# Optimization experiments

Measured on AMD Instinct MI355X. Metric: run time of the kernel, lower is better.

## Reference

```python
import jax, jax.numpy as jnp
import numpy as np

B, T, D, H = 8, 1024, 512, 8
QD, PD, POSD, VD, K = 32, 4, 48, 64, 31
FF = 4 * D
FF1, FF2, FF3, NLA = FF * 3 // 4, FF, FF * 5 // 4, D * 3 // 4


def _swoosh_l(x):
    return jax.nn.softplus(x - 4.0) - 0.08 * x - 0.035


def _swoosh_r(x):
    return jax.nn.softplus(x - 1.0) - 0.08 * x - 0.313261687


def setup_inputs() -> dict:
    key = jax.random.key(0)
    ks = iter(jax.random.split(key, 64))

    def w(shape, fan_in):
        return jax.random.normal(next(ks), shape, jnp.float32) * (fan_in ** -0.5)

    inp = {
        'x': jax.random.normal(next(ks), (B, T, D), jnp.float32),
        'pos_emb': jax.random.normal(next(ks), (2 * T - 1, POSD), jnp.float32),
        'mask': jnp.ones((B, T), bool),
        'attw_q_w': w((D, H * QD), D), 'attw_k_w': w((D, H * QD), D),
        'attw_pq_w': w((D, H * PD), D), 'attw_pos_w': w((POSD, H * PD), POSD),
        'ff1_in_w': w((D, FF1), D), 'ff1_in_b': jnp.zeros(FF1),
        'ff1_out_w': w((FF1, D), FF1), 'ff1_out_b': jnp.zeros(D),
        'nla_w': w((D, NLA * 3), D), 'nla_b': jnp.zeros(NLA * 3),
        'nla_out_w': w((NLA, D), NLA), 'nla_out_b': jnp.zeros(D),
        'sa1_v_w': w((D, H * VD), D), 'sa1_v_b': jnp.zeros(H * VD),
        'sa1_o_w': w((H * VD, D), H * VD), 'sa1_o_b': jnp.zeros(D),
        'conv1_in_w': w((D, 2 * D), D), 'conv1_in_b': jnp.zeros(2 * D),
        'conv1_dw_w': w((D, 1, K), K), 'conv1_dw_b': jnp.zeros(D),
        'conv1_out_w': w((D, D), D), 'conv1_out_b': jnp.zeros(D),
        'ff2_in_w': w((D, FF2), D), 'ff2_in_b': jnp.zeros(FF2),
        'ff2_out_w': w((FF2, D), FF2), 'ff2_out_b': jnp.zeros(D),
        'mid_scale': jax.random.uniform(next(ks), (D,), jnp.float32),
        'sa2_v_w': w((D, H * VD), D), 'sa2_v_b': jnp.zeros(H * VD),
        'sa2_o_w': w((H * VD, D), H * VD), 'sa2_o_b': jnp.zeros(D),
        'conv2_in_w': w((D, 2 * D), D), 'conv2_in_b': jnp.zeros(2 * D),
        'conv2_dw_w': w((D, 1, K), K), 'conv2_dw_b': jnp.zeros(D),
        'conv2_out_w': w((D, D), D), 'conv2_out_b': jnp.zeros(D),
        'ff3_in_w': w((D, FF3), D), 'ff3_in_b': jnp.zeros(FF3),
        'ff3_out_w': w((FF3, D), FF3), 'ff3_out_b': jnp.zeros(D),
        'norm_bias': jnp.zeros(D), 'norm_log_scale': jnp.zeros(()),
        'out_scale': jax.random.uniform(next(ks), (D,), jnp.float32),
    }
    return inp


def _forward(x, pos_emb, attw_q_w, attw_k_w, attw_pq_w, attw_pos_w,
             ff1_in_w, ff1_in_b, ff1_out_w, ff1_out_b,
             nla_w, nla_b, nla_out_w, nla_out_b,
             sa1_v_w, sa1_v_b, sa1_o_w, sa1_o_b,
             conv1_in_w, conv1_in_b, conv1_dw_w, conv1_dw_b, conv1_out_w, conv1_out_b,
             ff2_in_w, ff2_in_b, ff2_out_w, ff2_out_b,
             mid_scale,
             sa2_v_w, sa2_v_b, sa2_o_w, sa2_o_b,
             conv2_in_w, conv2_in_b, conv2_dw_w, conv2_dw_b, conv2_out_w, conv2_out_b,
             ff3_in_w, ff3_in_b, ff3_out_w, ff3_out_b,
             norm_bias, norm_log_scale, out_scale, mask):
    res = x
    # --- relative-pos multi-head attention weights ---
    q = (x @ attw_q_w).reshape(B, T, H, QD).transpose(0, 2, 1, 3)
    k = (x @ attw_k_w).reshape(B, T, H, QD).transpose(0, 2, 1, 3)
    p = (x @ attw_pq_w).reshape(B, T, H, PD).transpose(0, 2, 1, 3)
    content = jnp.einsum('bhtd,bhsd->bhts', q, k) * (QD ** -0.5)
    rel = (pos_emb @ attw_pos_w).reshape(2 * T - 1, H, PD).transpose(1, 0, 2)
    idx = jnp.arange(T)[:, None] - jnp.arange(T)[None, :] + (T - 1)
    relg = rel[:, idx]  # [H, T, T, PD]
    scores = content + jnp.einsum('bhtd,htsd->bhts', p, relg)
    scores = jnp.where(mask[:, None, None, :], scores, -10000.0)
    attn = jax.nn.softmax(scores, axis=-1)
    attn = jnp.where(mask[:, None, :, None], attn, 0.0)

    def mk(y):
        return jnp.where(mask[..., None], y, 0.0)

    def ff(y, wi, bi, wo, bo):
        return _swoosh_l(y @ wi + bi) @ wo + bo

    def sa(y, vw, vb, ow, ob):
        v = (y @ vw + vb).reshape(B, T, H, VD).transpose(0, 2, 1, 3)
        o = jnp.einsum('bhts,bhsd->bhtd', attn, v).transpose(0, 2, 1, 3).reshape(B, T, H * VD)
        return o @ ow + ob

    def conv(y, iw, ib, dw, db, ow, ob):
        u = y @ iw + ib
        a, g = jnp.split(u, 2, axis=-1)
        a = (a * jax.nn.sigmoid(g)).transpose(0, 2, 1)  # [B, D, T]
        a = jnp.where(mask[:, None, :], a, 0.0)
        c = jax.lax.conv_general_dilated(a, dw, (1,), [(K // 2, K // 2)],
                                         dimension_numbers=('NCH', 'OIH', 'NCH'),
                                         feature_group_count=D) + db[None, :, None]
        c = _swoosh_r(c.transpose(0, 2, 1))
        return mk(c @ ow + ob)

    def bypass(r, u, s):
        s = jnp.clip(s, 0.2, 1.0)  # eval/steady regime
        return r + (u - r) * s

    x = mk(x + ff(x, ff1_in_w, ff1_in_b, ff1_out_w, ff1_out_b))
    # non-linear attention (uses head 0)
    a, b, c = jnp.split(x @ nla_w + nla_b, 3, axis=-1)
    att0 = jnp.einsum('bts,bsd->btd', attn[:, 0], jnp.tanh(b) * c)
    x = mk(x + ((a * att0) @ nla_out_w + nla_out_b))
    x = mk(x + sa(x, sa1_v_w, sa1_v_b, sa1_o_w, sa1_o_b))
    x = mk(x + conv(x, conv1_in_w, conv1_in_b, conv1_dw_w, conv1_dw_b, conv1_out_w, conv1_out_b))
    x = mk(x + ff(x, ff2_in_w, ff2_in_b, ff2_out_w, ff2_out_b))
    x = mk(bypass(res, x, mid_scale))
    x = mk(x + sa(x, sa2_v_w, sa2_v_b, sa2_o_w, sa2_o_b))
    x = mk(x + conv(x, conv2_in_w, conv2_in_b, conv2_dw_w, conv2_dw_b, conv2_out_w, conv2_out_b))
    x = mk(x + ff(x, ff3_in_w, ff3_in_b, ff3_out_w, ff3_out_b))
    # BiasNorm
    rms = jnp.sqrt(jnp.mean((x - norm_bias) ** 2, axis=-1, keepdims=True) + 1e-8)
    x = x / rms * jnp.exp(norm_log_scale)
    x = mk(bypass(res, x, out_scale))
    return x


def reference(x, pos_emb, mask, attw_q_w, attw_k_w, attw_pq_w, attw_pos_w,
              ff1_in_w, ff1_in_b, ff1_out_w, ff1_out_b,
              nla_w, nla_b, nla_out_w, nla_out_b,
              sa1_v_w, sa1_v_b, sa1_o_w, sa1_o_b,
              conv1_in_w, conv1_in_b, conv1_dw_w, conv1_dw_b, conv1_out_w, conv1_out_b,
              ff2_in_w, ff2_in_b, ff2_out_w, ff2_out_b,
              mid_scale,
              sa2_v_w, sa2_v_b, sa2_o_w, sa2_o_b,
              conv2_in_w, conv2_in_b, conv2_dw_w, conv2_dw_b, conv2_out_w, conv2_out_b,
              ff3_in_w, ff3_in_b, ff3_out_w, ff3_out_b,
              norm_bias, norm_log_scale, out_scale):
    return _forward(x, pos_emb, attw_q_w, attw_k_w, attw_pq_w, attw_pos_w,
                    ff1_in_w, ff1_in_b, ff1_out_w, ff1_out_b,
                    nla_w, nla_b, nla_out_w, nla_out_b,
                    sa1_v_w, sa1_v_b, sa1_o_w, sa1_o_b,
                    conv1_in_w, conv1_in_b, conv1_dw_w, conv1_dw_b, conv1_out_w, conv1_out_b,
                    ff2_in_w, ff2_in_b, ff2_out_w, ff2_out_b,
                    mid_scale,
                    sa2_v_w, sa2_v_b, sa2_o_w, sa2_o_b,
                    conv2_in_w, conv2_in_b, conv2_dw_w, conv2_dw_b, conv2_out_w, conv2_out_b,
                    ff3_in_w, ff3_in_b, ff3_out_w, ff3_out_b,
                    norm_bias, norm_log_scale, out_scale, mask)
```

## Files before the change

kernel.cpp:

```cpp
#include <hip/hip_runtime.h>
#include <hip/hip_bf16.h>
#include <math.h>

using bf16 = __hip_bfloat16;
using f16 = _Float16;
typedef short s16x8 __attribute__((ext_vector_type(8)));
typedef f16   f16x2 __attribute__((ext_vector_type(2)));
typedef float f32x4 __attribute__((ext_vector_type(4)));
typedef unsigned int u32;
#define DEV __device__ __forceinline__
#define AS1 __attribute__((address_space(1)))
#define AS3 __attribute__((address_space(3)))

constexpr int Bc = 8, Tc = 1024, Dc = 512, Hc = 8;
constexpr int QDc = 32, PDc = 4, POSDc = 48, VDc = 64;
constexpr int Nrow = Bc * Tc;
constexpr int KWc = 31;

DEV float frcp(float x) { return __builtin_amdgcn_rcpf(x); }
DEV float softplus_f(float y) { return fmaxf(y, 0.f) + __logf(1.f + __expf(-fabsf(y))); }
DEV float swoosh_l_f(float x) { return softplus_f(x - 4.f) - 0.08f * x - 0.035f; }
DEV float swoosh_r_f(float x) { return softplus_f(x - 1.f) - 0.08f * x - 0.313261687f; }
DEV float sigmoid_f(float x)  { return frcp(1.f + __expf(-x)); }
DEV float tanh_f(float x) {
// ... 9 lines not shown
DEV u32 packbf(float a, float b) {
  return ((u32)(unsigned short)f2bb(b) << 16) | (u32)(unsigned short)f2bb(a);
}
DEV float dot2(u32 a, u32 b, float c) {
#if __has_builtin(__builtin_amdgcn_fdot2)
  union { u32 u; f16x2 v; } x, y; x.u = a; y.u = b;
  return __builtin_amdgcn_fdot2(x.v, y.v, c, false);
#else
  return c + h2f(a & 0xffff) * h2f(b & 0xffff) + h2f(a >> 16) * h2f(b >> 16);
#endif
}

DEV float wave_max(float v) {
#pragma unroll
  for (int o = 32; o > 0; o >>= 1) v = fmaxf(v, __shfl_xor(v, o));
  return v;
}
DEV float wave_sum(float v) {
#pragma unroll
  for (int o = 32; o > 0; o >>= 1) v += __shfl_xor(v, o);
  return v;
}

DEV void gload16(const void* g, void* l) {
  __builtin_amdgcn_global_load_lds((const AS1 u32*)g, (AS3 u32*)l, 16, 0, 0);
}

#define SWZ(a) ((a) ^ ((((a) >> 7) & 7) << 4))

template <int ACT, int WM, int WN, int FM, int FN>
__global__ __launch_bounds__(256) void gemm_mfma(
    const bf16* __restrict__ A, const bf16* __restrict__ B,
    const float* __restrict__ bias, const float* __restrict__ resid,
    float* __restrict__ Cf, bf16* __restrict__ Cb,
    int M, int N, int K, int lda, int ldb, int ldc,
    long sAz, long sBo, long sBi, long sCo, long sCi, int nh) {
  constexpr int BM = WM * FM * 16, BN = WN * FN * 16;
  constexpr int ASZ = BM * 128, BUF = (BM + BN) * 128;
  constexpr int LPS = BM / 32 + BN / 32;

  int z = blockIdx.z;
  int zo = z / nh, zi = z - zo * nh;
  A += (long)z * sAz;
  B += (long)zo * sBo + (long)zi * sBi;
  long coff = (long)zo * sCo + (long)zi * sCi;

  __shared__ char lds[2 * BUF];

  int tid = threadIdx.x;
  int lane = tid & 63, w = tid >> 6;
  int wm = w / WN, wn = w % WN;

  int gx = gridDim.x;
  int nwg = gx * gridDim.y;
  int flat = blockIdx.y * gx + blockIdx.x;
  if ((nwg & 7) == 0) flat = (flat & 7) * (nwg >> 3) + (flat >> 3);
  int m0 = (flat / gx) * BM, n0 = (flat % gx) * BN;

  int lrow = lane >> 3, lch = lane & 7;
  const bf16* ga = A + (long)(m0 + w * (BM / 4) + lrow) * lda + ((lch ^ lrow) << 3);
  const bf16* gb = B + (long)(n0 + w * (BN / 4) + lrow) * ldb + ((lch ^ lrow) << 3);

  f32x4 acc[FM][FN];
#pragma unroll
  for (int i = 0; i < FM; ++i)
#pragma unroll
    for (int j = 0; j < FN; ++j) acc[i][j] = 0.f;

  int nt = K >> 6;
  {
    char* la = lds + w * (BM / 4) * 128;
    char* lb = lds + ASZ + w * (BN / 4) * 128;
#pragma unroll
    for (int i = 0; i < BM / 32; ++i) gload16(ga + (long)(i * 8) * lda, la + i * 1024);
#pragma unroll
    for (int i = 0; i < BN / 32; ++i) gload16(gb + (long)(i * 8) * ldb, lb + i * 1024);
  }

  for (int t = 0; t < nt; ++t) {
    char* cA = lds + (t & 1) * BUF;
    char* cB = cA + ASZ;
    if (t + 1 < nt) {
      int k0 = (t + 1) << 6;
      char* la = lds + ((t + 1) & 1) * BUF + w * (BM / 4) * 128;
      char* lb = lds + ((t + 1) & 1) * BUF + ASZ + w * (BN / 4) * 128;
#pragma unroll
      for (int i = 0; i < BM / 32; ++i) gload16(ga + (long)(i * 8) * lda + k0, la + i * 1024);
#pragma unroll
      for (int i = 0; i < BN / 32; ++i) gload16(gb + (long)(i * 8) * ldb + k0, lb + i * 1024);
      asm volatile("s_waitcnt vmcnt(%0)" :: "n"(LPS) : "memory");
    } else {
      asm volatile("s_waitcnt vmcnt(0)" ::: "memory");
    }
    __builtin_amdgcn_s_barrier();
    __builtin_amdgcn_sched_barrier(0);
#pragma unroll
    for (int ks = 0; ks < 2; ++ks) {
      int cg = ks * 4 + (lane >> 4);
      s16x8 af[FM], bfr[FN];
#pragma unroll
      for (int f = 0; f < FM; ++f) {
        int row = wm * FM * 16 + f * 16 + (lane & 15);
        af[f] = *(const s16x8*)(cA + row * 128 + ((cg ^ (row & 7)) << 4));
      }
#pragma unroll
      for (int f = 0; f < FN; ++f) {
        int row = wn * FN * 16 + f * 16 + (lane & 15);
        bfr[f] = *(const s16x8*)(cB + row * 128 + ((cg ^ (row & 7)) << 4));
      }
#pragma unroll
      for (int fm = 0; fm < FM; ++fm)
#pragma unroll
        for (int fn = 0; fn < FN; ++fn)
          acc[fm][fn] = __builtin_amdgcn_mfma_f32_16x16x32_bf16(
              af[fm], bfr[fn], acc[fm][fn], 0, 0, 0);
    }
    __builtin_amdgcn_sched_barrier(0);
    __builtin_amdgcn_s_barrier();
  }

  int rbase = m0 + wm * FM * 16 + (lane >> 4) * 4;
  int cbase = n0 + wn * FN * 16 + (lane & 15);
#pragma unroll
  for (int fn = 0; fn < FN; ++fn) {
    int col = cbase + fn * 16;
    if (col >= N) continue;
    float bv = bias ? bias[col] : 0.f;
#pragma unroll
    for (int fm = 0; fm < FM; ++fm) {
#pragma unroll
      for (int r = 0; r < 4; ++r) {
        int row = rbase + fm * 16 + r;
        if (row >= M) continue;
        float v = acc[fm][fn][r] + bv;
        if (ACT == 1) v = swoosh_l_f(v);
        long ci = coff + (long)row * ldc + col;
        if (resid) v += resid[ci];
        if (Cf) Cf[ci] = v;
        if (Cb) Cb[ci] = __float2bfloat16(v);
      }
    }
  }
}

__global__ __launch_bounds__(256) void gemm_mfma_nt(
    const bf16* __restrict__ A, const bf16* __restrict__ B,
    bf16* __restrict__ Cb, int M, int N, int K, int lda, int ldb, int ldc,
    long sAz, long sBo, long sCo) {
  int z = blockIdx.z;
  A += (long)z * sAz;
  B += (long)z * sBo;
  long coff = (long)z * sCo;

  __shared__ char lds[32768];
  char* Al = lds;
  char* Bl = lds + 16384;

  int tid = threadIdx.x;
  int lane = tid & 63, w = tid >> 6;
  int wm = w >> 1, wn = w & 1;
  int m0 = blockIdx.y * 128, n0 = blockIdx.x * 128;

  f32x4 acc[4][4];
#pragma unroll
  for (int i = 0; i < 4; ++i)
#pragma unroll
    for (int j = 0; j < 4; ++j) acc[i][j] = 0.f;

  for (int k0 = 0; k0 < K; k0 += 64) {
#pragma unroll
    for (int i = 0; i < 4; ++i) {
      int flat = tid + i * 256;
// ... 164 lines not shown
  for (int e = 0; e < 8; ++e) o1[e] = t[q * 16 + 8 + e][j];
  short* dp = (short*)dst + (long)(by + j) * R + bx + q * 16;
  *(s16x8*)dp = o0;
  *(s16x8*)(dp + 8) = o1;
}

__global__ void dw_transpose_kernel(const float* __restrict__ dw1, float* __restrict__ o1,
                                    const float* __restrict__ dw2, float* __restrict__ o2) {
  int i = blockIdx.x * 256 + threadIdx.x;
  if (i >= 2 * 512 * KWc) return;
  const float* s = (i < 512 * KWc) ? dw1 : dw2;
  float* o = (i < 512 * KWc) ? o1 : o2;
  int j = (i < 512 * KWc) ? i : i - 512 * KWc;
  int d = j / KWc, kk = j - d * KWc;
  o[kk * 512 + d] = s[j];
}

__global__ void f2b_kernel(const float* __restrict__ in, bf16* __restrict__ out, int nOct) {
  int i = blockIdx.x * 256 + threadIdx.x;
  if (i >= nOct) return;
  float4 a = *(const float4*)(in + (long)i * 8);
  float4 b = *(const float4*)(in + (long)i * 8 + 4);
  s16x8 o;
  o[0] = f2bb(a.x); o[1] = f2bb(a.y); o[2] = f2bb(a.z); o[3] = f2bb(a.w);
  o[4] = f2bb(b.x); o[5] = f2bb(b.y); o[6] = f2bb(b.z); o[7] = f2bb(b.w);
  *(s16x8*)((short*)out + (long)i * 8) = o;
}

__global__ __launch_bounds__(256) void scores_softmax_fused(
    const bf16* __restrict__ qk, const f16* __restrict__ ph,
    const float* __restrict__ rel, bf16* __restrict__ attn) {
  int bh = blockIdx.y;
  int h = bh & (Hc - 1), b = bh >> 3;
  int t0 = blockIdx.x * 32;
  int tid = threadIdx.x, lane = tid & 63, w = tid >> 6;
  int wr = w >> 1, wc = w & 1;

  __shared__ unsigned short scS[32 * 1024];
  __shared__ u32 rel01[1056], rel23[1056];
  __shared__ u32 pS[32][2];
  __shared__ float mS[32][2], lS[32][2];

  for (int i = tid; i < 1055; i += 256) {
    float4 rv = *(const float4*)(rel + (long)(t0 + i) * 32 + h * 4);
    rel01[i] = ((u32)f2h(rv.y) << 16) | f2h(rv.x);
    rel23[i] = ((u32)f2h(rv.w) << 16) | f2h(rv.z);
  }
  if (tid < 32) {
    const u32* pp = (const u32*)(ph + ((long)(b * Tc + t0 + tid)) * 32 + h * 4);
    pS[tid][0] = pp[0]; pS[tid][1] = pp[1];
  }

  s16x8 af = *(const s16x8*)(qk + ((long)(b * Tc + t0 + wr * 16 + (lane & 15))) * 512 +
                             h * QDc + (lane >> 4) * 8);
  int g = lane >> 4;
  int r0 = wr * 16 + g * 4;
  float mx[4] = {-3e38f, -3e38f, -3e38f, -3e38f};
  f32x4 zero = {0.f, 0.f, 0.f, 0.f};
#pragma unroll 4
  for (int tile = 0; tile < 32; ++tile) {
    int s0 = wc * 512 + tile * 16;
    s16x8 bfr = *(const s16x8*)(qk + ((long)(b * Tc + s0 + (lane & 15))) * 512 +
                                256 + h * QDc + (lane >> 4) * 8);
    f32x4 acc = __builtin_amdgcn_mfma_f32_16x16x32_bf16(af, bfr, zero, 0, 0, 0);
    int scol = s0 + (lane & 15);
#pragma unroll
    for (int r = 0; r < 4; ++r) {
      float v = acc[r];
      mx[r] = fmaxf(mx[r], v);
      int trow = r0 + r;
      int byteoff = trow * 2048 + ((scol * 2) ^ (((trow >> 2) & 3) << 5));
      *(unsigned short*)((char*)scS + byteoff) = f2h(v);
    }
  }
#pragma unroll
  for (int o = 1; o < 16; o <<= 1)
#pragma unroll
    for (int r = 0; r < 4; ++r) mx[r] = fmaxf(mx[r], __shfl_xor(mx[r], o));
  if ((lane & 15) == 0) {
#pragma unroll
    for (int r = 0; r < 4; ++r) mS[r0 + r][wc] = mx[r];
  }
  __syncthreads();

  for (int r = 0; r < 16; ++r) {
    int trow = wr * 16 + r;
    float mf = fmaxf(mS[trow][0], mS[trow][1]);
    u32 p01 = pS[trow][0], p23 = pS[trow][1];
    int mask = ((trow >> 2) & 3) << 5;
    char* rowbase = (char*)scS + trow * 2048;
    float lsum = 0.f;
#pragma unroll
    for (int i = 0; i < 4; ++i) {
      int byteoff = (wc * 1024 + lane * 4 + i * 256) ^ mask;
      u32 cw = *(u32*)(rowbase + byteoff);
      int scol0 = wc * 512 + (lane + i * 64) * 2;
      int i0 = trow - scol0 + 1023;
      float pos0 = dot2(p23, rel23[i0],     dot2(p01, rel01[i0],     0.f));
      float pos1 = dot2(p23, rel23[i0 - 1], dot2(p01, rel01[i0 - 1], 0.f));
      float e0 = __expf(h2f(cw & 0xffff) + pos0 - mf);
      float e1 = __expf(h2f(cw >> 16)    + pos1 - mf);
      lsum += e0 + e1;
      *(u32*)(rowbase + byteoff) = packbf(e0, e1);
    }
    lsum = wave_sum(lsum);
    if (lane == 0) lS[trow][wc] = lsum;
  }
  __syncthreads();

  for (int r = 0; r < 16; ++r) {
    int trow = wr * 16 + r;
    float inv = frcp(lS[trow][0] + lS[trow][1]);
    int mask = ((trow >> 2) & 3) << 5;
    char* rowbase = (char*)scS + trow * 2048;
    u32* grow = (u32*)(attn + ((long)bh * Tc + t0 + trow) * Tc) + wc * 256;
#pragma unroll
    for (int i = 0; i < 4; ++i) {
      int byteoff = (wc * 1024 + lane * 4 + i * 256) ^ mask;
      u32 ew = *(u32*)(rowbase + byteoff);
      grow[lane + i * 64] = packbf(b2f((short)(ew & 0xffff)) * inv,
                                   b2f((short)(ew >> 16)) * inv);
    }
  }
}

__global__ void glu_kernel(const bf16* __restrict__ u, bf16* __restrict__ out, int nOct) {
  int i = blockIdx.x * 256 + threadIdx.x;
  if (i >= nOct) return;
  int row = i >> 6, oct = i & 63;
  const short* ur = (const short*)u + (long)row * 1024;
  s16x8 av = *(const s16x8*)(ur + oct * 8);
  s16x8 gv = *(const s16x8*)(ur + 512 + oct * 8);
  s16x8 o;
#pragma unroll
  for (int j = 0; j < 8; ++j) o[j] = f2bb(b2f(av[j]) * sigmoid_f(b2f(gv[j])));
  *(s16x8*)((short*)out + (long)row * 512 + oct * 8) = o;
}

__global__ void tanhmul_kernel(const bf16* __restrict__ abc, bf16* __restrict__ out, int nOct) {
  int i = blockIdx.x * 256 + threadIdx.x;
  if (i >= nOct) return;
  int row = i / 48, oct = i - row * 48;
  const short* r = (const short*)abc + (long)row * 1152;
  s16x8 bv = *(const s16x8*)(r + 384 + oct * 8);
  s16x8 cv = *(const s16x8*)(r + 768 + oct * 8);
  s16x8 o;
#pragma unroll
  for (int j = 0; j < 8; ++j) o[j] = f2bb(tanh_f(b2f(bv[j])) * b2f(cv[j]));
  *(s16x8*)((short*)out + (long)row * 384 + oct * 8) = o;
}

__global__ void amul_kernel(const bf16* __restrict__ abc, bf16* __restrict__ io, int nOct) {
  int i = blockIdx.x * 256 + threadIdx.x;
  if (i >= nOct) return;
  int row = i / 48, oct = i - row * 48;
  const short* r = (const short*)abc + (long)row * 1152;
  s16x8 av = *(const s16x8*)(r + oct * 8);
  short* p = (short*)io + (long)row * 384 + oct * 8;
  s16x8 v = *(const s16x8*)p;
#pragma unroll
  for (int j = 0; j < 8; ++j) v[j] = f2bb(b2f(v[j]) * b2f(av[j]));
  *(s16x8*)p = v;
}

__global__ void bypass_kernel(const float* __restrict__ r, const float* __restrict__ u,
                              const float* __restrict__ s, float* __restrict__ out,
                              bf16* __restrict__ outb, int nOct) {
  int i = blockIdx.x * 256 + threadIdx.x;
  if (i >= nOct) return;
  int d0 = (i & 63) * 8;
  long base = (long)i * 8;
  float4 r0 = *(const float4*)(r + base), r1 = *(const float4*)(r + base + 4);
  float4 u0 = *(const float4*)(u + base), u1 = *(const float4*)(u + base + 4);
  float4 s0 = *(const float4*)(s + d0),  s1 = *(const float4*)(s + d0 + 4);
  float4 o0, o1;
  o0.x = r0.x + (u0.x - r0.x) * clip_s(s0.x);
  o0.y = r0.y + (u0.y - r0.y) * clip_s(s0.y);
  o0.z = r0.z + (u0.z - r0.z) * clip_s(s0.z);
  o0.w = r0.w + (u0.w - r0.w) * clip_s(s0.w);
  o1.x = r1.x + (u1.x - r1.x) * clip_s(s1.x);
  o1.y = r1.y + (u1.y - r1.y) * clip_s(s1.y);
  o1.z = r1.z + (u1.z - r1.z) * clip_s(s1.z);
  o1.w = r1.w + (u1.w - r1.w) * clip_s(s1.w);
  *(float4*)(out + base) = o0;
  *(float4*)(out + base + 4) = o1;
  s16x8 ob;
  ob[0] = f2bb(o0.x); ob[1] = f2bb(o0.y); ob[2] = f2bb(o0.z); ob[3] = f2bb(o0.w);
  ob[4] = f2bb(o1.x); ob[5] = f2bb(o1.y); ob[6] = f2bb(o1.z); ob[7] = f2bb(o1.w);
  *(s16x8*)((short*)outb + base) = ob;
}

// ... 27 lines not shown
  *(s16x8*)((short*)c + (long)bt * 512 + oct * 8) = o;
}

__global__ __launch_bounds__(256) void rmsnorm_bypass_kernel(
    const float* __restrict__ x, const float* __restrict__ x0,
    const float* __restrict__ nb, const float* __restrict__ nls,
    const float* __restrict__ os, float* __restrict__ out) {
  int row = blockIdx.x;
  int tid = threadIdx.x;
  const float* xr = x + (long)row * 512;
  const float* rr = x0 + (long)row * 512;
  float* orow = out + (long)row * 512;
  float v0 = xr[tid], v1 = xr[tid + 256];
  float d0 = v0 - nb[tid], d1 = v1 - nb[tid + 256];
  float ss = d0 * d0 + d1 * d1;
  __shared__ float red[4];
  int lane = tid & 63, wid = tid >> 6;
  ss = wave_sum(ss);
  if (lane == 0) red[wid] = ss;
  __syncthreads();
  ss = red[0] + red[1] + red[2] + red[3];
  float rms = sqrtf(ss * (1.f / 512.f) + 1e-8f);
  float scl = expf(nls[0]) / rms;
  float r0 = rr[tid], s0 = clip_s(os[tid]);
  orow[tid] = r0 + (v0 * scl - r0) * s0;
  float r1 = rr[tid + 256], s1 = clip_s(os[tid + 256]);
  orow[tid + 256] = r1 + (v1 * scl - r1) * s1;
}

static inline int cdiv(int a, int b) { return (a + b - 1) / b; }

template <int ACT, int WM = 2, int WN = 2, int FM = 2, int FN = 2>
static void mfma_launch(hipStream_t st, const bf16* A, const bf16* B, const float* bias,
                        const float* resid, float* Cf, bf16* Cb,
                        int M, int N, int K, int lda, int ldb, int ldc,
                        int Z = 1, int nh = 1, long sAz = 0, long sBo = 0, long sBi = 0,
                        long sCo = 0, long sCi = 0) {
  dim3 grid(cdiv(N, WN * FN * 16), cdiv(M, WM * FM * 16), Z);
  gemm_mfma<ACT, WM, WN, FM, FN><<<grid, dim3(256), 0, st>>>(
      A, B, bias, resid, Cf, Cb, M, N, K, lda, ldb, ldc,
      sAz, sBo, sBi, sCo, sCi, nh);
}
#define MFMA_AV 4, 1, 2, 4

extern "C" void kernel_launch(void* const* d_in, const int* in_sizes, int n_in,
                              void* d_out, int out_size, void* d_ws, size_t ws_size,
                              hipStream_t stream) {
  const float* x0        = (const float*)d_in[0];
  const float* pos_emb   = (const float*)d_in[1];
  const float* Wq        = (const float*)d_in[3];
  const float* Wk        = (const float*)d_in[4];
  const float* Wpq       = (const float*)d_in[5];
  const float* Wpos      = (const float*)d_in[6];
  const float* ff1_in_w  = (const float*)d_in[7];
  const float* ff1_in_b  = (const float*)d_in[8];
  const float* ff1_out_w = (const float*)d_in[9];
  const float* ff1_out_b = (const float*)d_in[10];
  const float* nla_w     = (const float*)d_in[11];
  const float* nla_b     = (const float*)d_in[12];
  const float* nla_out_w = (const float*)d_in[13];
  const float* nla_out_b = (const float*)d_in[14];
  const float* sa1_v_w   = (const float*)d_in[15];
  const float* sa1_v_b   = (const float*)d_in[16];
  const float* sa1_o_w   = (const float*)d_in[17];
  const float* sa1_o_b   = (const float*)d_in[18];
  const float* cv1_in_w  = (const float*)d_in[19];
  const float* cv1_in_b  = (const float*)d_in[20];
  const float* cv1_dw_w  = (const float*)d_in[21];
  const float* cv1_dw_b  = (const float*)d_in[22];
  const float* cv1_out_w = (const float*)d_in[23];
  const float* cv1_out_b = (const float*)d_in[24];
  const float* ff2_in_w  = (const float*)d_in[25];
  const float* ff2_in_b  = (const float*)d_in[26];
// ... 4 lines not shown
  const float* sa2_v_b   = (const float*)d_in[31];
  const float* sa2_o_w   = (const float*)d_in[32];
  const float* sa2_o_b   = (const float*)d_in[33];
  const float* cv2_in_w  = (const float*)d_in[34];
  const float* cv2_in_b  = (const float*)d_in[35];
  const float* cv2_dw_w  = (const float*)d_in[36];
  const float* cv2_dw_b  = (const float*)d_in[37];
  const float* cv2_out_w = (const float*)d_in[38];
  const float* cv2_out_b = (const float*)d_in[39];
  const float* ff3_in_w  = (const float*)d_in[40];
  const float* ff3_in_b  = (const float*)d_in[41];
  const float* ff3_out_w = (const float*)d_in[42];
  const float* ff3_out_b = (const float*)d_in[43];
  const float* norm_bias = (const float*)d_in[44];
  const float* nls       = (const float*)d_in[45];
  const float* out_scale = (const float*)d_in[46];
  float* out = (float*)d_out;

  char* wsb = (char*)d_ws;
  size_t off = 0;
  bf16* attn  = (bf16*)(wsb + off); off += (size_t)Bc * Hc * Tc * Tc * 2;
  float* xA   = (float*)(wsb + off); off += (size_t)Nrow * Dc * 4;
  float* xB   = (float*)(wsb + off); off += (size_t)Nrow * Dc * 4;
  bf16*  xb   = (bf16*)(wsb + off);  off += (size_t)Nrow * Dc * 2;
  bf16*  x0b  = (bf16*)(wsb + off);  off += (size_t)Nrow * Dc * 2;
  bf16*  big1b = (bf16*)(wsb + off); off += (size_t)Nrow * 2560 * 2;
  bf16*  big2b = (bf16*)(wsb + off); off += (size_t)Nrow * Dc * 2;
  bf16*  wT    = (bf16*)(wsb + off); off += (size_t)9961472 * 2;
  float* dwT1  = (float*)(wsb + off); off += (size_t)KWc * 512 * 4;
  float* dwT2  = (float*)(wsb + off); off += (size_t)KWc * 512 * 4;
  bf16* big3b = big1b + (size_t)Nrow * 2048;
  bf16* vT    = big2b;
  bf16* qk    = big1b;
  f16*  ph    = (f16*)(big1b + (size_t)Nrow * 512);
  float* relb = (float*)(ph + (size_t)Nrow * 32);

  bf16* p_w = wT;
  auto alloc_w = [&](int n, int k) { bf16* r = p_w; p_w += (size_t)n * k; return r; };
  bf16* ff1_in_wT  = alloc_w(1536, 512);
  bf16* ff1_out_wT = alloc_w(512, 1536);
  bf16* nla_wT     = alloc_w(1152, 512);
  bf16* nla_out_wT = alloc_w(512, 384);
  bf16* sa1_v_wT   = alloc_w(512, 512);
  bf16* sa1_o_wT   = alloc_w(512, 512);
  bf16* cv1_in_wT  = alloc_w(1024, 512);
  bf16* cv1_out_wT = alloc_w(512, 512);
  bf16* ff2_in_wT  = alloc_w(2048, 512);
  bf16* ff2_out_wT = alloc_w(512, 2048);
  bf16* sa2_v_wT   = alloc_w(512, 512);
  bf16* sa2_o_wT   = alloc_w(512, 512);
  bf16* cv2_in_wT  = alloc_w(1024, 512);
  bf16* cv2_out_wT = alloc_w(512, 512);
  bf16* ff3_in_wT  = alloc_w(2560, 512);
  bf16* ff3_out_wT = alloc_w(512, 2560);
  bf16* WqkT       = alloc_w(512, 512);

  const int nOctD  = Nrow * 64;
  const int nOct384 = Nrow * 48;

  f2b_kernel<<<cdiv(nOctD, 256), 256, 0, stream>>>(x0, x0b, nOctD);
  {
    TBatch tb{};
    auto add = [&](int idx, const float* s, bf16* d, int K, int N, int& t0, float sc) {
      tb.d[idx] = {s, d, K, N, t0, cdiv(N, 32), sc};
      t0 += cdiv(N, 32) * cdiv(K, 32);
    };
    int t0 = 0;
    add(0,  ff1_in_w,  ff1_in_wT,  512, 1536, t0, 1.f);
    add(1,  ff1_out_w, ff1_out_wT, 1536, 512, t0, 1.f);
    add(2,  nla_w,     nla_wT,     512, 1152, t0, 1.f);
    add(3,  nla_out_w, nla_out_wT, 384, 512,  t0, 1.f);
    add(4,  sa1_v_w,   sa1_v_wT,   512, 512,  t0, 1.f);
    add(5,  sa1_o_w,   sa1_o_wT,   512, 512,  t0, 1.f);
    add(6,  cv1_in_w,  cv1_in_wT,  512, 1024, t0, 1.f);
    add(7,  cv1_out_w, cv1_out_wT, 512, 512,  t0, 1.f);
    add(8,  ff2_in_w,  ff2_in_wT,  512, 2048, t0, 1.f);
    add(9,  ff2_out_w, ff2_out_wT, 2048, 512, t0, 1.f);
    add(10, sa2_v_w,   sa2_v_wT,   512, 512,  t0, 1.f);
    add(11, sa2_o_w,   sa2_o_wT,   512, 512,  t0, 1.f);
    add(12, cv2_in_w,  cv2_in_wT,  512, 1024, t0, 1.f);
    add(13, cv2_out_w, cv2_out_wT, 512, 512,  t0, 1.f);
    add(14, ff3_in_w,  ff3_in_wT,  512, 2560, t0, 1.f);
    add(15, ff3_out_w, ff3_out_wT, 2560, 512, t0, 1.f);
    add(16, Wq,        WqkT,       512, 256,  t0, 0.17677669529663687f);
    add(17, Wk,        WqkT + (size_t)256 * 512, 512, 256, t0, 1.f);
    tb.n = 18;
    transpose_batch_kernel<<<t0, 256, 0, stream>>>(tb);
  }
  dw_transpose_kernel<<<cdiv(2 * 512 * KWc, 256), 256, 0, stream>>>(
      cv1_dw_w, dwT1, cv2_dw_w, dwT2);

  gemm_tile_f32<<<dim3(1, cdiv(2 * Tc - 1, 64)), 256, 0, stream>>>(
      pos_emb, Wpos, relb, nullptr, 2 * Tc - 1, 32, POSDc, POSDc, 32, 32);
  gemm_tile_f32<<<dim3(1, cdiv(Nrow, 64)), 256, 0, stream>>>(
      x0, Wpq, nullptr, ph, Nrow, 32, Dc, Dc, 32, 32);
  mfma_launch<0>(stream, x0b, WqkT, nullptr, nullptr, nullptr, qk,
                 Nrow, 512, 512, 512, 512, 512);
  scores_softmax_fused<<<dim3(Tc / 32, 64), 256, 0, stream>>>(qk, ph, relb, attn);

  mfma_launch<1>(stream, x0b, ff1_in_wT, ff1_in_b, nullptr, nullptr, big1b,
                 Nrow, 1536, 512, 512, 512, 1536);
  mfma_launch<0>(stream, big1b, ff1_out_wT, ff1_out_b, x0, xA, xb,
                 Nrow, 512, 1536, 1536, 1536, 512);

  mfma_launch<0>(stream, xb, nla_wT, nla_b, nullptr, nullptr, big1b,
                 Nrow, 1152, 512, 512, 512, 1152);
  tanhmul_kernel<<<cdiv(nOct384, 256), 256, 0, stream>>>(big1b, big2b, nOct384);
  {
    dim3 grid(cdiv(384, 128), cdiv(Tc, 128), Bc);
    gemm_mfma_nt<<<grid, dim3(256), 0, stream>>>(
        attn, big2b, big3b, Tc, 384, Tc, Tc, 384, 384,
        (long)Hc * Tc * Tc, (long)Tc * 384, (long)Tc * 384);
  }
  amul_kernel<<<cdiv(nOct384, 256), 256, 0, stream>>>(big1b, big3b, nOct384);
  mfma_launch<0>(stream, big3b, nla_out_wT, nla_out_b, xA, xB, xb,
                 Nrow, 512, 384, 384, 384, 512);

  mfma_launch<0>(stream, xb, sa1_v_wT, sa1_v_b, nullptr, nullptr, big3b,
                 Nrow, 512, 512, 512, 512, 512);
  transpose_bf16_kernel<<<dim3(Nrow / 64, 8), 256, 0, stream>>>(big3b, vT, Nrow, 512);
  mfma_launch<0, MFMA_AV>(stream, attn, vT, nullptr, nullptr, nullptr, big3b,
                          Tc, VDc, Tc, Tc, Nrow, 512,
                          Bc * Hc, Hc, (long)Tc * Tc, Tc, (long)VDc * Nrow,
                          (long)Tc * 512, VDc);
  mfma_launch<0>(stream, big3b, sa1_o_wT, sa1_o_b, xB, xA, xb,
                 Nrow, 512, 512, 512, 512, 512);

  mfma_launch<0>(stream, xb, cv1_in_wT, cv1_in_b, nullptr, nullptr, big1b,
                 Nrow, 1024, 512, 512, 512, 1024);
  glu_kernel<<<cdiv(nOctD, 256), 256, 0, stream>>>(big1b, big2b, nOctD);
  dwconv_kernel<<<cdiv(nOctD, 256), 256, 0, stream>>>(big2b, dwT1, cv1_dw_b, big3b);
  mfma_launch<0>(stream, big3b, cv1_out_wT, cv1_out_b, xA, xB, xb,
                 Nrow, 512, 512, 512, 512, 512);

  mfma_launch<1>(stream, xb, ff2_in_wT, ff2_in_b, nullptr, nullptr, big1b,
                 Nrow, 2048, 512, 512, 512, 2048);
  mfma_launch<0>(stream, big1b, ff2_out_wT, ff2_out_b, xB, xA, nullptr,
                 Nrow, 512, 2048, 2048, 2048, 512);

  bypass_kernel<<<cdiv(nOctD, 256), 256, 0, stream>>>(x0, xA, mid_scale, xB, xb, nOctD);

  mfma_launch<0>(stream, xb, sa2_v_wT, sa2_v_b, nullptr, nullptr, big3b,
                 Nrow, 512, 512, 512, 512, 512);
  transpose_bf16_kernel<<<dim3(Nrow / 64, 8), 256, 0, stream>>>(big3b, vT, Nrow, 512);
  mfma_launch<0, MFMA_AV>(stream, attn, vT, nullptr, nullptr, nullptr, big3b,
                          Tc, VDc, Tc, Tc, Nrow, 512,
                          Bc * Hc, Hc, (long)Tc * Tc, Tc, (long)VDc * Nrow,
                          (long)Tc * 512, VDc);
  mfma_launch<0>(stream, big3b, sa2_o_wT, sa2_o_b, xB, xA, xb,
                 Nrow, 512, 512, 512, 512, 512);

  mfma_launch<0>(stream, xb, cv2_in_wT, cv2_in_b, nullptr, nullptr, big1b,
                 Nrow, 1024, 512, 512, 512, 1024);
  glu_kernel<<<cdiv(nOctD, 256), 256, 0, stream>>>(big1b, big2b, nOctD);
  dwconv_kernel<<<cdiv(nOctD, 256), 256, 0, stream>>>(big2b, dwT2, cv2_dw_b, big3b);
  mfma_launch<0>(stream, big3b, cv2_out_wT, cv2_out_b, xA, xB, xb,
                 Nrow, 512, 512, 512, 512, 512);

  mfma_launch<1>(stream, xb, ff3_in_wT, ff3_in_b, nullptr, nullptr, big1b,
                 Nrow, 2560, 512, 512, 512, 2560);
  mfma_launch<0>(stream, big1b, ff3_out_wT, ff3_out_b, xB, xA, nullptr,
                 Nrow, 512, 2560, 2560, 2560, 512);

  rmsnorm_bypass_kernel<<<Nrow, 256, 0, stream>>>(xA, x0, norm_bias, nls, out_scale, out);
}
```

Before: 855.4 us.

## Fuse GLU and tanh-mul into multi-panel GEMM epilogues; restructure scores softmax

The GEMM template gains multi-panel modes that load two or three weight column panels and compute their accumulators together. The GLU gate and the tanh(b)*c product are then applied in the epilogue, which removes the separate glu and tanhmul kernels and the wide intermediate round trip through memory. The scores_softmax kernel now handles 16 rows per block and adds the positional term during the score pass, and it keeps the exp values in registers instead of doing a second LDS pass. The cost is more LDS and registers per GEMM block, which may lower occupancy, and twice as many softmax blocks.

```diff
diff --git a/kernel.cpp b/kernel.cpp
--- a/kernel.cpp
+++ b/kernel.cpp
@@ -65,12 +65,14 @@
 __global__ __launch_bounds__(256) void gemm_mfma(
     const bf16* __restrict__ A, const bf16* __restrict__ B,
     const float* __restrict__ bias, const float* __restrict__ resid,
-    float* __restrict__ Cf, bf16* __restrict__ Cb,
+    float* __restrict__ Cf, bf16* __restrict__ Cb, bf16* __restrict__ Cb2,
     int M, int N, int K, int lda, int ldb, int ldc,
     long sAz, long sBo, long sBi, long sCo, long sCi, int nh) {
   constexpr int BM = WM * FM * 16, BN = WN * FN * 16;
-  constexpr int ASZ = BM * 128, BUF = (BM + BN) * 128;
-  constexpr int LPS = BM / 32 + BN / 32;
+  constexpr int NP = (ACT == 2) ? 2 : (ACT == 3) ? 3 : 1;
+  constexpr int PANOFF = (ACT == 2) ? 512 : 384;
+  constexpr int ASZ = BM * 128, BUF = (BM + NP * BN) * 128;
+  constexpr int LPS = BM / 32 + NP * (BN / 32);
 
   int z = blockIdx.z;
   int zo = z / nh, zi = z - zo * nh;
@@ -94,33 +96,43 @@
   const bf16* ga = A + (long)(m0 + w * (BM / 4) + lrow) * lda + ((lch ^ lrow) << 3);
   const bf16* gb = B + (long)(n0 + w * (BN / 4) + lrow) * ldb + ((lch ^ lrow) << 3);
 
-  f32x4 acc[FM][FN];
-#pragma unroll
-  for (int i = 0; i < FM; ++i)
-#pragma unroll
-    for (int j = 0; j < FN; ++j) acc[i][j] = 0.f;
+  f32x4 acc[NP][FM][FN];
+#pragma unroll
+  for (int p = 0; p < NP; ++p)
+#pragma unroll
+    for (int i = 0; i < FM; ++i)
+#pragma unroll
+      for (int j = 0; j < FN; ++j) acc[p][i][j] = 0.f;
 
   int nt = K >> 6;
   {
     char* la = lds + w * (BM / 4) * 128;
-    char* lb = lds + ASZ + w * (BN / 4) * 128;
 #pragma unroll
     for (int i = 0; i < BM / 32; ++i) gload16(ga + (long)(i * 8) * lda, la + i * 1024);
 #pragma unroll
-    for (int i = 0; i < BN / 32; ++i) gload16(gb + (long)(i * 8) * ldb, lb + i * 1024);
+    for (int p = 0; p < NP; ++p) {
+      const bf16* gp = gb + (long)(p * PANOFF) * ldb;
+      char* lb = lds + ASZ + p * BN * 128 + w * (BN / 4) * 128;
+#pragma unroll
+      for (int i = 0; i < BN / 32; ++i) gload16(gp + (long)(i * 8) * ldb, lb + i * 1024);
+    }
   }
 
   for (int t = 0; t < nt; ++t) {
     char* cA = lds + (t & 1) * BUF;
-    char* cB = cA + ASZ;
     if (t + 1 < nt) {
       int k0 = (t + 1) << 6;
-      char* la = lds + ((t + 1) & 1) * BUF + w * (BM / 4) * 128;
-      char* lb = lds + ((t + 1) & 1) * BUF + ASZ + w * (BN / 4) * 128;
+      char* base = lds + ((t + 1) & 1) * BUF;
+      char* la = base + w * (BM / 4) * 128;
 #pragma unroll
       for (int i = 0; i < BM / 32; ++i) gload16(ga + (long)(i * 8) * lda + k0, la + i * 1024);
 #pragma unroll
-      for (int i = 0; i < BN / 32; ++i) gload16(gb + (long)(i * 8) * ldb + k0, lb + i * 1024);
+      for (int p = 0; p < NP; ++p) {
+        const bf16* gp = gb + (long)(p * PANOFF) * ldb;
+        char* lb = base + ASZ + p * BN * 128 + w * (BN / 4) * 128;
+#pragma unroll
+        for (int i = 0; i < BN / 32; ++i) gload16(gp + (long)(i * 8) * ldb + k0, lb + i * 1024);
+      }
       asm volatile("s_waitcnt vmcnt(%0)" :: "n"(LPS) : "memory");
     } else {
       asm volatile("s_waitcnt vmcnt(0)" ::: "memory");
@@ -130,23 +142,28 @@
 #pragma unroll
     for (int ks = 0; ks < 2; ++ks) {
       int cg = ks * 4 + (lane >> 4);
-      s16x8 af[FM], bfr[FN];
+      s16x8 af[FM];
 #pragma unroll
       for (int f = 0; f < FM; ++f) {
         int row = wm * FM * 16 + f * 16 + (lane & 15);
         af[f] = *(const s16x8*)(cA + row * 128 + ((cg ^ (row & 7)) << 4));
       }
 #pragma unroll
-      for (int f = 0; f < FN; ++f) {
-        int row = wn * FN * 16 + f * 16 + (lane & 15);
-        bfr[f] = *(const s16x8*)(cB + row * 128 + ((cg ^ (row & 7)) << 4));
+      for (int p = 0; p < NP; ++p) {
+        char* cB = cA + ASZ + p * BN * 128;
+        s16x8 bfr[FN];
+#pragma unroll
+        for (int f = 0; f < FN; ++f) {
+          int row = wn * FN * 16 + f * 16 + (lane & 15);
+          bfr[f] = *(const s16x8*)(cB + row * 128 + ((cg ^ (row & 7)) << 4));
+        }
+#pragma unroll
+        for (int fm = 0; fm < FM; ++fm)
+#pragma unroll
+          for (int fn = 0; fn < FN; ++fn)
+            acc[p][fm][fn] = __builtin_amdgcn_mfma_f32_16x16x32_bf16(
+                af[fm], bfr[fn], acc[p][fm][fn], 0, 0, 0);
       }
-#pragma unroll
-      for (int fm = 0; fm < FM; ++fm)
-#pragma unroll
-        for (int fn = 0; fn < FN; ++fn)
-          acc[fm][fn] = __builtin_amdgcn_mfma_f32_16x16x32_bf16(
-              af[fm], bfr[fn], acc[fm][fn], 0, 0, 0);
     }
     __builtin_amdgcn_sched_barrier(0);
     __builtin_amdgcn_s_barrier();
@@ -165,12 +182,24 @@
       for (int r = 0; r < 4; ++r) {
         int row = rbase + fm * 16 + r;
         if (row >= M) continue;
-        float v = acc[fm][fn][r] + bv;
-        if (ACT == 1) v = swoosh_l_f(v);
         long ci = coff + (long)row * ldc + col;
-        if (resid) v += resid[ci];
-        if (Cf) Cf[ci] = v;
-        if (Cb) Cb[ci] = __float2bfloat16(v);
+        if constexpr (ACT == 2) {
+          float va = acc[0][fm][fn][r] + bv;
+          float vg = acc[1][fm][fn][r] + bias[col + 512];
+          Cb[ci] = __float2bfloat16(va * sigmoid_f(vg));
+        } else if constexpr (ACT == 3) {
+          float va = acc[0][fm][fn][r] + bv;
+          float vb = acc[1][fm][fn][r] + bias[col + 384];
+          float vc = acc[2][fm][fn][r] + bias[col + 768];
+          Cb2[ci] = __float2bfloat16(va);
+          Cb[ci] = __float2bfloat16(tanh_f(vb) * vc);
+        } else {
+          float v = acc[0][fm][fn][r] + bv;
+          if (ACT == 1) v = swoosh_l_f(v);
+          if (resid) v += resid[ci];
+          if (Cf) Cf[ci] = v;
+          if (Cb) Cb[ci] = __float2bfloat16(v);
+        }
       }
     }
   }
@@ -401,45 +430,49 @@
     const float* __restrict__ rel, bf16* __restrict__ attn) {
   int bh = blockIdx.y;
   int h = bh & (Hc - 1), b = bh >> 3;
-  int t0 = blockIdx.x * 32;
+  int t0 = blockIdx.x * 16;
   int tid = threadIdx.x, lane = tid & 63, w = tid >> 6;
-  int wr = w >> 1, wc = w & 1;
-
-  __shared__ unsigned short scS[32 * 1024];
-  __shared__ u32 rel01[1056], rel23[1056];
-  __shared__ u32 pS[32][2];
-  __shared__ float mS[32][2], lS[32][2];
-
-  for (int i = tid; i < 1055; i += 256) {
+
+  __shared__ unsigned short scS[16 * 1024];
+  __shared__ u32 rel01[1040], rel23[1040];
+  __shared__ u32 pS[16][2];
+  __shared__ float mS[16][4];
+
+  for (int i = tid; i < 1039; i += 256) {
     float4 rv = *(const float4*)(rel + (long)(t0 + i) * 32 + h * 4);
     rel01[i] = ((u32)f2h(rv.y) << 16) | f2h(rv.x);
     rel23[i] = ((u32)f2h(rv.w) << 16) | f2h(rv.z);
   }
-  if (tid < 32) {
+  if (tid < 16) {
     const u32* pp = (const u32*)(ph + ((long)(b * Tc + t0 + tid)) * 32 + h * 4);
     pS[tid][0] = pp[0]; pS[tid][1] = pp[1];
   }
-
-  s16x8 af = *(const s16x8*)(qk + ((long)(b * Tc + t0 + wr * 16 + (lane & 15))) * 512 +
+  __syncthreads();
+
+  s16x8 af = *(const s16x8*)(qk + ((long)(b * Tc + t0 + (lane & 15))) * 512 +
                              h * QDc + (lane >> 4) * 8);
   int g = lane >> 4;
-  int r0 = wr * 16 + g * 4;
+  u32 p01[4], p23[4];
+#pragma unroll
+  for (int r = 0; r < 4; ++r) { p01[r] = pS[g * 4 + r][0]; p23[r] = pS[g * 4 + r][1]; }
   float mx[4] = {-3e38f, -3e38f, -3e38f, -3e38f};
   f32x4 zero = {0.f, 0.f, 0.f, 0.f};
+  int cols0 = w * 256;
 #pragma unroll 4
-  for (int tile = 0; tile < 32; ++tile) {
-    int s0 = wc * 512 + tile * 16;
+  for (int tile = 0; tile < 16; ++tile) {
+    int s0 = cols0 + tile * 16;
     s16x8 bfr = *(const s16x8*)(qk + ((long)(b * Tc + s0 + (lane & 15))) * 512 +
                                 256 + h * QDc + (lane >> 4) * 8);
     f32x4 acc = __builtin_amdgcn_mfma_f32_16x16x32_bf16(af, bfr, zero, 0, 0, 0);
     int scol = s0 + (lane & 15);
+    int idx0 = g * 4 - scol + 1023;
 #pragma unroll
     for (int r = 0; r < 4; ++r) {
-      float v = acc[r];
+      int idx = idx0 + r;
+      float pos = dot2(p23[r], rel23[idx], dot2(p01[r], rel01[idx], 0.f));
+      float v = acc[r] + pos;
       mx[r] = fmaxf(mx[r], v);
-      int trow = r0 + r;
-      int byteoff = trow * 2048 + ((scol * 2) ^ (((trow >> 2) & 3) << 5));
-      *(unsigned short*)((char*)scS + byteoff) = f2h(v);
+      *(unsigned short*)((char*)scS + (g * 4 + r) * 2048 + ((scol * 2) ^ (g << 5))) = f2h(v);
     }
   }
 #pragma unroll
@@ -448,84 +481,40 @@
     for (int r = 0; r < 4; ++r) mx[r] = fmaxf(mx[r], __shfl_xor(mx[r], o));
   if ((lane & 15) == 0) {
 #pragma unroll
-    for (int r = 0; r < 4; ++r) mS[r0 + r][wc] = mx[r];
+    for (int r = 0; r < 4; ++r) mS[g * 4 + r][w] = mx[r];
   }
   __syncthreads();
 
-  for (int r = 0; r < 16; ++r) {
-    int trow = wr * 16 + r;
-    float mf = fmaxf(mS[trow][0], mS[trow][1]);
-    u32 p01 = pS[trow][0], p23 = pS[trow][1];
-    int mask = ((trow >> 2) & 3) << 5;
-    char* rowbase = (char*)scS + trow * 2048;
+#pragma unroll
+  for (int rr = 0; rr < 4; ++rr) {
+    int row = w * 4 + rr;
+    float mf = fmaxf(fmaxf(mS[row][0], mS[row][1]), fmaxf(mS[row][2], mS[row][3]));
+    int mask = ((row >> 2) & 3) << 5;
+    char* rowbase = (char*)scS + row * 2048;
+    float e[16];
     float lsum = 0.f;
 #pragma unroll
-    for (int i = 0; i < 4; ++i) {
-      int byteoff = (wc * 1024 + lane * 4 + i * 256) ^ mask;
-      u32 cw = *(u32*)(rowbase + byteoff);
-      int scol0 = wc * 512 + (lane + i * 64) * 2;
-      int i0 = trow - scol0 + 1023;
-      float pos0 = dot2(p23, rel23[i0],     dot2(p01, rel01[i0],     0.f));
-      float pos1 = dot2(p23, rel23[i0 - 1], dot2(p01, rel01[i0 - 1], 0.f));
-      float e0 = __expf(h2f(cw & 0xffff) + pos0 - mf);
-      float e1 = __expf(h2f(cw >> 16)    + pos1 - mf);
+    for (int k = 0; k < 8; ++k) {
+      u32 cw = *(u32*)(rowbase + (((lane + k * 64) * 4) ^ mask));
+      float e0 = __expf(h2f(cw & 0xffff) - mf);
+      float e1 = __expf(h2f(cw >> 16) - mf);
+      e[k * 2] = e0; e[k * 2 + 1] = e1;
       lsum += e0 + e1;
-      *(u32*)(rowbase + byteoff) = packbf(e0, e1);
     }
     lsum = wave_sum(lsum);
-    if (lane == 0) lS[trow][wc] = lsum;
-  }
-  __syncthreads();
-
-  for (int r = 0; r < 16; ++r) {
-    int trow = wr * 16 + r;
-    float inv = frcp(lS[trow][0] + lS[trow][1]);
-    int mask = ((trow >> 2) & 3) << 5;
-    char* rowbase = (char*)scS + trow * 2048;
-    u32* grow = (u32*)(attn + ((long)bh * Tc + t0 + trow) * Tc) + wc * 256;
-#pragma unroll
-    for (int i = 0; i < 4; ++i) {
-      int byteoff = (wc * 1024 + lane * 4 + i * 256) ^ mask;
-      u32 ew = *(u32*)(rowbase + byteoff);
-      grow[lane + i * 64] = packbf(b2f((short)(ew & 0xffff)) * inv,
-                                   b2f((short)(ew >> 16)) * inv);
-    }
-  }
-}
-
-__global__ void glu_kernel(const bf16* __restrict__ u, bf16* __restrict__ out, int nOct) {
+    float inv = frcp(lsum);
+    u32* grow = (u32*)(attn + ((long)bh * Tc + t0 + row) * Tc);
+#pragma unroll
+    for (int k = 0; k < 8; ++k)
+      grow[lane + k * 64] = packbf(e[k * 2] * inv, e[k * 2 + 1] * inv);
+  }
+}
+
+__global__ void amul_kernel(const bf16* __restrict__ a, bf16* __restrict__ io, int nOct) {
   int i = blockIdx.x * 256 + threadIdx.x;
   if (i >= nOct) return;
-  int row = i >> 6, oct = i & 63;
-  const short* ur = (const short*)u + (long)row * 1024;
-  s16x8 av = *(const s16x8*)(ur + oct * 8);
-  s16x8 gv = *(const s16x8*)(ur + 512 + oct * 8);
-  s16x8 o;
-#pragma unroll
-  for (int j = 0; j < 8; ++j) o[j] = f2bb(b2f(av[j]) * sigmoid_f(b2f(gv[j])));
-  *(s16x8*)((short*)out + (long)row * 512 + oct * 8) = o;
-}
-
-__global__ void tanhmul_kernel(const bf16* __restrict__ abc, bf16* __restrict__ out, int nOct) {
-  int i = blockIdx.x * 256 + threadIdx.x;
-  if (i >= nOct) return;
-  int row = i / 48, oct = i - row * 48;
-  const short* r = (const short*)abc + (long)row * 1152;
-  s16x8 bv = *(const s16x8*)(r + 384 + oct * 8);
-  s16x8 cv = *(const s16x8*)(r + 768 + oct * 8);
-  s16x8 o;
-#pragma unroll
-  for (int j = 0; j < 8; ++j) o[j] = f2bb(tanh_f(b2f(bv[j])) * b2f(cv[j]));
-  *(s16x8*)((short*)out + (long)row * 384 + oct * 8) = o;
-}
-
-__global__ void amul_kernel(const bf16* __restrict__ abc, bf16* __restrict__ io, int nOct) {
-  int i = blockIdx.x * 256 + threadIdx.x;
-  if (i >= nOct) return;
-  int row = i / 48, oct = i - row * 48;
-  const short* r = (const short*)abc + (long)row * 1152;
-  s16x8 av = *(const s16x8*)(r + oct * 8);
-  short* p = (short*)io + (long)row * 384 + oct * 8;
+  s16x8 av = *(const s16x8*)((const short*)a + (long)i * 8);
+  short* p = (short*)io + (long)i * 8;
   s16x8 v = *(const s16x8*)p;
 #pragma unroll
   for (int j = 0; j < 8; ++j) v[j] = f2bb(b2f(v[j]) * b2f(av[j]));
@@ -619,13 +608,13 @@
 
 template <int ACT, int WM = 2, int WN = 2, int FM = 2, int FN = 2>
 static void mfma_launch(hipStream_t st, const bf16* A, const bf16* B, const float* bias,
-                        const float* resid, float* Cf, bf16* Cb,
+                        const float* resid, float* Cf, bf16* Cb, bf16* Cb2,
                         int M, int N, int K, int lda, int ldb, int ldc,
                         int Z = 1, int nh = 1, long sAz = 0, long sBo = 0, long sBi = 0,
                         long sCo = 0, long sCi = 0) {
   dim3 grid(cdiv(N, WN * FN * 16), cdiv(M, WM * FM * 16), Z);
   gemm_mfma<ACT, WM, WN, FM, FN><<<grid, dim3(256), 0, st>>>(
-      A, B, bias, resid, Cf, Cb, M, N, K, lda, ldb, ldc,
+      A, B, bias, resid, Cf, Cb, Cb2, M, N, K, lda, ldb, ldc,
       sAz, sBo, sBi, sCo, sCi, nh);
 }
 #define MFMA_AV 4, 1, 2, 4
@@ -696,6 +685,7 @@
   bf16* big3b = big1b + (size_t)Nrow * 2048;
   bf16* vT    = big2b;
   bf16* qk    = big1b;
+  bf16* abuf  = big1b;
   f16*  ph    = (f16*)(big1b + (size_t)Nrow * 512);
   float* relb = (float*)(ph + (size_t)Nrow * 32);
 
@@ -758,72 +748,69 @@
       pos_emb, Wpos, relb, nullptr, 2 * Tc - 1, 32, POSDc, POSDc, 32, 32);
   gemm_tile_f32<<<dim3(1, cdiv(Nrow, 64)), 256, 0, stream>>>(
       x0, Wpq, nullptr, ph, Nrow, 32, Dc, Dc, 32, 32);
-  mfma_launch<0>(stream, x0b, WqkT, nullptr, nullptr, nullptr, qk,
+  mfma_launch<0>(stream, x0b, WqkT, nullptr, nullptr, nullptr, qk, nullptr,
                  Nrow, 512, 512, 512, 512, 512);
-  scores_softmax_fused<<<dim3(Tc / 32, 64), 256, 0, stream>>>(qk, ph, relb, attn);
-
-  mfma_launch<1>(stream, x0b, ff1_in_wT, ff1_in_b, nullptr, nullptr, big1b,
+  scores_softmax_fused<<<dim3(Tc / 16, 64), 256, 0, stream>>>(qk, ph, relb, attn);
+
+  mfma_launch<1>(stream, x0b, ff1_in_wT, ff1_in_b, nullptr, nullptr, big1b, nullptr,
                  Nrow, 1536, 512, 512, 512, 1536);
-  mfma_launch<0>(stream, big1b, ff1_out_wT, ff1_out_b, x0, xA, xb,
+  mfma_launch<0>(stream, big1b, ff1_out_wT, ff1_out_b, x0, xA, xb, nullptr,
                  Nrow, 512, 1536, 1536, 1536, 512);
 
-  mfma_launch<0>(stream, xb, nla_wT, nla_b, nullptr, nullptr, big1b,
-                 Nrow, 1152, 512, 512, 512, 1152);
-  tanhmul_kernel<<<cdiv(nOct384, 256), 256, 0, stream>>>(big1b, big2b, nOct384);
+  mfma_launch<3>(stream, xb, nla_wT, nla_b, nullptr, nullptr, big2b, abuf,
+                 Nrow, 384, 512, 512, 512, 384);
   {
     dim3 grid(cdiv(384, 128), cdiv(Tc, 128), Bc);
     gemm_mfma_nt<<<grid, dim3(256), 0, stream>>>(
         attn, big2b, big3b, Tc, 384, Tc, Tc, 384, 384,
         (long)Hc * Tc * Tc, (long)Tc * 384, (long)Tc * 384);
   }
-  amul_kernel<<<cdiv(nOct384, 256), 256, 0, stream>>>(big1b, big3b, nOct384);
-  mfma_launch<0>(stream, big3b, nla_out_wT, nla_out_b, xA, xB, xb,
+  amul_kernel<<<cdiv(nOct384, 256), 256, 0, stream>>>(abuf, big3b, nOct384);
+  mfma_launch<0>(stream, big3b, nla_out_wT, nla_out_b, xA, xB, xb, nullptr,
                  Nrow, 512, 384, 384, 384, 512);
 
-  mfma_launch<0>(stream, xb, sa1_v_wT, sa1_v_b, nullptr, nullptr, big3b,
+  mfma_launch<0>(stream, xb, sa1_v_wT, sa1_v_b, nullptr, nullptr, big3b, nullptr,
                  Nrow, 512, 512, 512, 512, 512);
   transpose_bf16_kernel<<<dim3(Nrow / 64, 8), 256, 0, stream>>>(big3b, vT, Nrow, 512);
-  mfma_launch<0, MFMA_AV>(stream, attn, vT, nullptr, nullptr, nullptr, big3b,
+  mfma_launch<0, MFMA_AV>(stream, attn, vT, nullptr, nullptr, nullptr, big3b, nullptr,
                           Tc, VDc, Tc, Tc, Nrow, 512,
                           Bc * Hc, Hc, (long)Tc * Tc, Tc, (long)VDc * Nrow,
                           (long)Tc * 512, VDc);
-  mfma_launch<0>(stream, big3b, sa1_o_wT, sa1_o_b, xB, xA, xb,
+  mfma_launch<0>(stream, big3b, sa1_o_wT, sa1_o_b, xB, xA, xb, nullptr,
                  Nrow, 512, 512, 512, 512, 512);
 
-  mfma_launch<0>(stream, xb, cv1_in_wT, cv1_in_b, nullptr, nullptr, big1b,
-                 Nrow, 1024, 512, 512, 512, 1024);
-  glu_kernel<<<cdiv(nOctD, 256), 256, 0, stream>>>(big1b, big2b, nOctD);
+  mfma_launch<2>(stream, xb, cv1_in_wT, cv1_in_b, nullptr, nullptr, big2b, nullptr,
+                 Nrow, 512, 512, 512, 512, 512);
   dwconv_kernel<<<cdiv(nOctD, 256), 256, 0, stream>>>(big2b, dwT1, cv1_dw_b, big3b);
-  mfma_launch<0>(stream, big3b, cv1_out_wT, cv1_out_b, xA, xB, xb,
+  mfma_launch<0>(stream, big3b, cv1_out_wT, cv1_out_b, xA, xB, xb, nullptr,
                  Nrow, 512, 512, 512, 512, 512);
 
-  mfma_launch<1>(stream, xb, ff2_in_wT, ff2_in_b, nullptr, nullptr, big1b,
+  mfma_launch<1>(stream, xb, ff2_in_wT, ff2_in_b, nullptr, nullptr, big1b, nullptr,
                  Nrow, 2048, 512, 512, 512, 2048);
-  mfma_launch<0>(stream, big1b, ff2_out_wT, ff2_out_b, xB, xA, nullptr,
+  mfma_launch<0>(stream, big1b, ff2_out_wT, ff2_out_b, xB, xA, nullptr, nullptr,
                  Nrow, 512, 2048, 2048, 2048, 512);
 
   bypass_kernel<<<cdiv(nOctD, 256), 256, 0, stream>>>(x0, xA, mid_scale, xB, xb, nOctD);
 
-  mfma_launch<0>(stream, xb, sa2_v_wT, sa2_v_b, nullptr, nullptr, big3b,
+  mfma_launch<0>(stream, xb, sa2_v_wT, sa2_v_b, nullptr, nullptr, big3b, nullptr,
                  Nrow, 512, 512, 512, 512, 512);
   transpose_bf16_kernel<<<dim3(Nrow / 64, 8), 256, 0, stream>>>(big3b, vT, Nrow, 512);
-  mfma_launch<0, MFMA_AV>(stream, attn, vT, nullptr, nullptr, nullptr, big3b,
+  mfma_launch<0, MFMA_AV>(stream, attn, vT, nullptr, nullptr, nullptr, big3b, nullptr,
                           Tc, VDc, Tc, Tc, Nrow, 512,
                           Bc * Hc, Hc, (long)Tc * Tc, Tc, (long)VDc * Nrow,
                           (long)Tc * 512, VDc);
-  mfma_launch<0>(stream, big3b, sa2_o_wT, sa2_o_b, xB, xA, xb,
+  mfma_launch<0>(stream, big3b, sa2_o_wT, sa2_o_b, xB, xA, xb, nullptr,
                  Nrow, 512, 512, 512, 512, 512);
 
-  mfma_launch<0>(stream, xb, cv2_in_wT, cv2_in_b, nullptr, nullptr, big1b,
-                 Nrow, 1024, 512, 512, 512, 1024);
-  glu_kernel<<<cdiv(nOctD, 256), 256, 0, stream>>>(big1b, big2b, nOctD);
+  mfma_launch<2>(stream, xb, cv2_in_wT, cv2_in_b, nullptr, nullptr, big2b, nullptr,
+                 Nrow, 512, 512, 512, 512, 512);
   dwconv_kernel<<<cdiv(nOctD, 256), 256, 0, stream>>>(big2b, dwT2, cv2_dw_b, big3b);
-  mfma_launch<0>(stream, big3b, cv2_out_wT, cv2_out_b, xA, xB, xb,
+  mfma_launch<0>(stream, big3b, cv2_out_wT, cv2_out_b, xA, xB, xb, nullptr,
                  Nrow, 512, 512, 512, 512, 512);
 
-  mfma_launch<1>(stream, xb, ff3_in_wT, ff3_in_b, nullptr, nullptr, big1b,
+  mfma_launch<1>(stream, xb, ff3_in_wT, ff3_in_b, nullptr, nullptr, big1b, nullptr,
                  Nrow, 2560, 512, 512, 512, 2560);
-  mfma_launch<0>(stream, big1b, ff3_out_wT, ff3_out_b, xB, xA, nullptr,
+  mfma_launch<0>(stream, big1b, ff3_out_wT, ff3_out_b, xB, xA, nullptr, nullptr,
                  Nrow, 512, 2560, 2560, 2560, 512);
 
   rmsnorm_bypass_kernel<<<Nrow, 256, 0, stream>>>(xA, x0, norm_bias, nls, out_scale, out);
```

After: 814.7 us (median of 2 runs). 1.05x faster.
